# Kernel optimization log

Measured on AMD Instinct MI355X. Metric: run time of the kernel, lower is better.

## Reference

```python
import jax, jax.numpy as jnp
import numpy as np

SHIFT = 4
MARGIN = 0.15


def _shift_loss(f1, m1, f2, m2):
    # f1,f2: [B,C,H,W] float; m1,m2: [B,1,H,W] bool
    # Original repeats masks to C channels; broadcasting is equivalent,
    # but mask.sum over (1,2,3) then includes a factor of C.
    C = f1.shape[1]
    dists = []
    for i in range(2 * SHIFT + 1):
        off = -SHIFT + i
        f2r = jnp.roll(f2, off, axis=-1)
        m2r = jnp.roll(m2, off, axis=-1)
        mask = m1 & m2r                              # [B,1,H,W]
        diff = jnp.where(mask, f1 - f2r, 0.0)        # broadcast over C
        num = jnp.sum(diff * diff, axis=(1, 2, 3))   # ||.||_2^2
        den = C * jnp.sum(mask, axis=(1, 2, 3)).astype(f1.dtype) + 0.001
        dists.append(num / den)
    return jnp.min(jnp.stack(dists, axis=0), axis=0)  # min over 9 shifts -> [B]


def setup_inputs() -> dict:
    key = jax.random.key(0)
    ka, kp, kn, kma, kmp, kmn = jax.random.split(key, 6)
    B, C, H, W = 64, 16, 32, 512
    a = jax.random.normal(ka, (B, C, H, W), dtype=jnp.float32)
    p = jax.random.normal(kp, (B, C, H, W), dtype=jnp.float32)
    n = jax.random.normal(kn, (B, C, H, W), dtype=jnp.float32)
    ma = jax.random.bernoulli(kma, 0.8, (B, 1, H, W))
    mp = jax.random.bernoulli(kmp, 0.8, (B, 1, H, W))
    mn = jax.random.bernoulli(kmn, 0.8, (B, 1, H, W))
    return {"a": a, "p": p, "n": n, "ma": ma, "mp": mp, "mn": mn}


def reference(a, p, n, ma, mp, mn):
    ap_loss = _shift_loss(a, ma, p, mp)
    an_loss = _shift_loss(a, ma, n, mn)
    loss = jax.nn.relu(ap_loss - an_loss + MARGIN)
    return jnp.mean(loss)
```

## Files before the change

### kernel.cpp

```cpp
#include <hip/hip_runtime.h>

#define NB 64
#define NC 16
#define NH 32
#define NW 512
#define HW (NH * NW)
#define CHW (NC * HW)
#define NOFF 9
#define NCPB 4

#define WS_NUM_AP 0
#define WS_NUM_AN 576
#define WS_CNT_AP 1152
#define WS_CNT_AN 1728
#define WS_FLOATS 2304

__device__ __forceinline__ float wave_sum_f(float v) {
#pragma unroll
    for (int o = 32; o > 0; o >>= 1) v += __shfl_down(v, o, 64);
    return v;
}

__global__ __launch_bounds__(256, 4) void num_kernel(
    const float* __restrict__ a, const float* __restrict__ p,
    const float* __restrict__ n, const int* __restrict__ ma,
    const int* __restrict__ mp, const int* __restrict__ mn,
    float* __restrict__ ws)
{
    const int b    = blockIdx.z;
    const int pair = blockIdx.y & 1;
    const int cg   = blockIdx.y >> 1;
    const int tid  = blockIdx.x * 256 + threadIdx.x;
    const int pos0 = tid * 4;
    const int w0   = pos0 & (NW - 1);
    const int row  = pos0 - w0;
    const int idxm = row + ((w0 - 4) & (NW - 1));
    const int idxp = row + ((w0 + 4) & (NW - 1));

    const int* MA = ma + b * HW;
    const int* M2 = (pair ? mn : mp) + b * HW;
    int4 mav = *(const int4*)(MA + pos0);
    int4 mf0 = *(const int4*)(M2 + idxm);
    int4 mf1 = *(const int4*)(M2 + pos0);
    int4 mf2 = *(const int4*)(M2 + idxp);

    float m1f[4]  = {mav.x ? 1.f : 0.f, mav.y ? 1.f : 0.f,
                     mav.z ? 1.f : 0.f, mav.w ? 1.f : 0.f};
    float m2f[12] = {mf0.x ? 1.f : 0.f, mf0.y ? 1.f : 0.f, mf0.z ? 1.f : 0.f, mf0.w ? 1.f : 0.f,
                     mf1.x ? 1.f : 0.f, mf1.y ? 1.f : 0.f, mf1.z ? 1.f : 0.f, mf1.w ? 1.f : 0.f,
                     mf2.x ? 1.f : 0.f, mf2.y ? 1.f : 0.f, mf2.z ? 1.f : 0.f, mf2.w ? 1.f : 0.f};

    const float* A = a + (size_t)b * CHW + (size_t)cg * NCPB * HW;
    const float* F = (pair ? n : p) + (size_t)b * CHW + (size_t)cg * NCPB * HW;

    float sa2[4];
    float sf2[12];
    float crS[NOFF];
#pragma unroll
    for (int j = 0; j < 4; ++j) sa2[j] = 0.f;
#pragma unroll
    for (int k = 0; k < 12; ++k) sf2[k] = 0.f;
#pragma unroll
    for (int s = 0; s < NOFF; ++s) crS[s] = 0.f;

#pragma unroll 2
    for (int c = 0; c < NCPB; ++c) {
        const float* Ac = A + c * HW;
        const float* Fc = F + c * HW;

        float4 av4 = *(const float4*)(Ac + pos0);
        float fb[12];
        *(float4*)&fb[0] = *(const float4*)(Fc + idxm);
        *(float4*)&fb[4] = *(const float4*)(Fc + pos0);
        *(float4*)&fb[8] = *(const float4*)(Fc + idxp);
        float avr[4] = {av4.x, av4.y, av4.z, av4.w};

        float am[4], fm[12];
#pragma unroll
        for (int j = 0; j < 4; ++j) am[j] = avr[j] * m1f[j];
#pragma unroll
        for (int k = 0; k < 12; ++k) fm[k] = fb[k] * m2f[k];

#pragma unroll
        for (int j = 0; j < 4; ++j) sa2[j] = fmaf(am[j], am[j], sa2[j]);
#pragma unroll
        for (int k = 0; k < 12; ++k) sf2[k] = fmaf(fm[k], fm[k], sf2[k]);
#pragma unroll
        for (int s = 0; s < NOFF; ++s) {
#pragma unroll
            for (int j = 0; j < 4; ++j) {
                crS[s] = fmaf(am[j], fm[j + 8 - s], crS[s]);
            }
        }
    }

    float sx[NOFF], cxf[NOFF];
#pragma unroll
    for (int s = 0; s < NOFF; ++s) {
        float t = 0.f, cc = 0.f;
#pragma unroll
        for (int j = 0; j < 4; ++j) {
            const int k = j + 8 - s;
            t  = fmaf(m2f[k], sa2[j], t);
            t  = fmaf(m1f[j], sf2[k], t);
            cc = fmaf(m1f[j], m2f[k], cc);
        }
        sx[s]  = fmaf(-2.f, crS[s], t);
        cxf[s] = cc;
    }

    __shared__ float red[4][20];
    const int lane = threadIdx.x & 63;
    const int wid  = threadIdx.x >> 6;

#pragma unroll
    for (int s = 0; s < NOFF; ++s) sx[s] = wave_sum_f(sx[s]);
    if (cg == 0) {
#pragma unroll
        for (int s = 0; s < NOFF; ++s) cxf[s] = wave_sum_f(cxf[s]);
    }
    if (lane == 0) {
#pragma unroll
        for (int s = 0; s < NOFF; ++s) {
            red[wid][s] = sx[s];
            red[wid][9 + s] = cxf[s];
        }
    }
    __syncthreads();

    float* numws = ws + (pair ? WS_NUM_AN : WS_NUM_AP) + b * NOFF;
    float* cntws = ws + (pair ? WS_CNT_AN : WS_CNT_AP) + b * NOFF;
    const int i = threadIdx.x;
    if (i < 9) {
        float v = red[0][i] + red[1][i] + red[2][i] + red[3][i];
        atomicAdd(numws + i, v);
    } else if (i < 18 && cg == 0) {
        float v = red[0][i] + red[1][i] + red[2][i] + red[3][i];
        atomicAdd(cntws + (i - 9), v);
    }
}

__global__ void finish_kernel(const float* __restrict__ ws, float* __restrict__ out)
{
    const int b = threadIdx.x;
    const float* num_ap = ws + WS_NUM_AP;
    const float* num_an = ws + WS_NUM_AN;
    const float* cnt_ap = ws + WS_CNT_AP;
    const float* cnt_an = ws + WS_CNT_AN;

    float ap = 3.4e38f, an = 3.4e38f;
#pragma unroll
    for (int s = 0; s < NOFF; ++s) {
        ap = fminf(ap, num_ap[b * NOFF + s] / (16.f * cnt_ap[b * NOFF + s] + 0.001f));
        an = fminf(an, num_an[b * NOFF + s] / (16.f * cnt_an[b * NOFF + s] + 0.001f));
    }
    float loss = fmaxf(ap - an + 0.15f, 0.f);
    loss = wave_sum_f(loss);
    if (b == 0) out[0] = loss * (1.0f / 64.f);
}

extern "C" void kernel_launch(void* const* d_in, const int* in_sizes, int n_in,
                              void* d_out, int out_size, void* d_ws, size_t ws_size,
                              hipStream_t stream) {
    const float* a = (const float*)d_in[0];
    const float* p = (const float*)d_in[1];
    const float* n = (const float*)d_in[2];
    const int* ma = (const int*)d_in[3];
    const int* mp = (const int*)d_in[4];
    const int* mn = (const int*)d_in[5];
    float* ws = (float*)d_ws;
    float* out = (float*)d_out;

    hipMemsetAsync(d_ws, 0, WS_FLOATS * sizeof(float), stream);

    num_kernel<<<dim3(16, 8, NB), 256, 0, stream>>>(a, p, n, ma, mp, mn, ws);
    finish_kernel<<<1, 64, 0, stream>>>(ws, out);
}
```

Baseline: 209.5 us.

## Map one wave per row and share shift halos via lane shuffles

Each wave now processes a full image row with eight contiguous elements per lane. The ±4 shift neighbourhood is obtained from adjacent lanes through shuffles instead of extra overlapping global loads of the second feature map and mask. This cuts redundant memory requests and halves the grid, at the cost of more registers per thread and added shuffle instructions.

```diff
diff --git a/kernel.cpp b/kernel.cpp
--- a/kernel.cpp
+++ b/kernel.cpp
@@ -30,36 +30,31 @@
     const int b    = blockIdx.z;
     const int pair = blockIdx.y & 1;
     const int cg   = blockIdx.y >> 1;
-    const int tid  = blockIdx.x * 256 + threadIdx.x;
-    const int pos0 = tid * 4;
-    const int w0   = pos0 & (NW - 1);
-    const int row  = pos0 - w0;
-    const int idxm = row + ((w0 - 4) & (NW - 1));
-    const int idxp = row + ((w0 + 4) & (NW - 1));
+    const int lane = threadIdx.x & 63;
+    const int wid  = threadIdx.x >> 6;
+    const int row  = blockIdx.x * 4 + wid;
+    const int base = row * NW + lane * 8;
+    const int prevL = (lane + 63) & 63;
+    const int nextL = (lane + 1)  & 63;
 
-    const int* MA = ma + b * HW;
-    const int* M2 = (pair ? mn : mp) + b * HW;
-    int4 mav = *(const int4*)(MA + pos0);
-    int4 mf0 = *(const int4*)(M2 + idxm);
-    int4 mf1 = *(const int4*)(M2 + pos0);
-    int4 mf2 = *(const int4*)(M2 + idxp);
+    const int* MA = ma + b * HW + base;
+    const int* M2 = (pair ? mn : mp) + b * HW + base;
+    int4 ma0 = *(const int4*)(MA);
+    int4 ma1 = *(const int4*)(MA + 4);
+    int4 mb0 = *(const int4*)(M2);
+    int4 mb1 = *(const int4*)(M2 + 4);
 
-    float m1f[4]  = {mav.x ? 1.f : 0.f, mav.y ? 1.f : 0.f,
-                     mav.z ? 1.f : 0.f, mav.w ? 1.f : 0.f};
-    float m2f[12] = {mf0.x ? 1.f : 0.f, mf0.y ? 1.f : 0.f, mf0.z ? 1.f : 0.f, mf0.w ? 1.f : 0.f,
-                     mf1.x ? 1.f : 0.f, mf1.y ? 1.f : 0.f, mf1.z ? 1.f : 0.f, mf1.w ? 1.f : 0.f,
-                     mf2.x ? 1.f : 0.f, mf2.y ? 1.f : 0.f, mf2.z ? 1.f : 0.f, mf2.w ? 1.f : 0.f};
+    float m1f[8] = {ma0.x ? 1.f : 0.f, ma0.y ? 1.f : 0.f, ma0.z ? 1.f : 0.f, ma0.w ? 1.f : 0.f,
+                    ma1.x ? 1.f : 0.f, ma1.y ? 1.f : 0.f, ma1.z ? 1.f : 0.f, ma1.w ? 1.f : 0.f};
+    float m2f[8] = {mb0.x ? 1.f : 0.f, mb0.y ? 1.f : 0.f, mb0.z ? 1.f : 0.f, mb0.w ? 1.f : 0.f,
+                    mb1.x ? 1.f : 0.f, mb1.y ? 1.f : 0.f, mb1.z ? 1.f : 0.f, mb1.w ? 1.f : 0.f};
 
-    const float* A = a + (size_t)b * CHW + (size_t)cg * NCPB * HW;
-    const float* F = (pair ? n : p) + (size_t)b * CHW + (size_t)cg * NCPB * HW;
+    const float* A = a + (size_t)b * CHW + (size_t)cg * NCPB * HW + base;
+    const float* F = (pair ? n : p) + (size_t)b * CHW + (size_t)cg * NCPB * HW + base;
 
-    float sa2[4];
-    float sf2[12];
-    float crS[NOFF];
+    float sa2[8], sf2[8], crS[NOFF];
 #pragma unroll
-    for (int j = 0; j < 4; ++j) sa2[j] = 0.f;
-#pragma unroll
-    for (int k = 0; k < 12; ++k) sf2[k] = 0.f;
+    for (int j = 0; j < 8; ++j) { sa2[j] = 0.f; sf2[j] = 0.f; }
 #pragma unroll
     for (int s = 0; s < NOFF; ++s) crS[s] = 0.f;
 
@@ -67,31 +62,50 @@
     for (int c = 0; c < NCPB; ++c) {
         const float* Ac = A + c * HW;
         const float* Fc = F + c * HW;
+        float4 a0 = *(const float4*)(Ac);
+        float4 a1 = *(const float4*)(Ac + 4);
+        float4 f0 = *(const float4*)(Fc);
+        float4 f1 = *(const float4*)(Fc + 4);
+        float av[8] = {a0.x, a0.y, a0.z, a0.w, a1.x, a1.y, a1.z, a1.w};
+        float fv[8] = {f0.x, f0.y, f0.z, f0.w, f1.x, f1.y, f1.z, f1.w};
 
-        float4 av4 = *(const float4*)(Ac + pos0);
-        float fb[12];
-        *(float4*)&fb[0] = *(const float4*)(Fc + idxm);
-        *(float4*)&fb[4] = *(const float4*)(Fc + pos0);
-        *(float4*)&fb[8] = *(const float4*)(Fc + idxp);
-        float avr[4] = {av4.x, av4.y, av4.z, av4.w};
+        float am[8], fm[8];
+#pragma unroll
+        for (int j = 0; j < 8; ++j) { am[j] = av[j] * m1f[j]; fm[j] = fv[j] * m2f[j]; }
 
-        float am[4], fm[12];
+        float wfm[16];
 #pragma unroll
-        for (int j = 0; j < 4; ++j) am[j] = avr[j] * m1f[j];
+        for (int i = 0; i < 4; ++i) wfm[i]      = __shfl(fm[4 + i], prevL, 64);
 #pragma unroll
-        for (int k = 0; k < 12; ++k) fm[k] = fb[k] * m2f[k];
+        for (int i = 0; i < 8; ++i) wfm[4 + i]  = fm[i];
+#pragma unroll
+        for (int i = 0; i < 4; ++i) wfm[12 + i] = __shfl(fm[i], nextL, 64);
 
 #pragma unroll
-        for (int j = 0; j < 4; ++j) sa2[j] = fmaf(am[j], am[j], sa2[j]);
+        for (int j = 0; j < 8; ++j) sa2[j] = fmaf(am[j], am[j], sa2[j]);
 #pragma unroll
-        for (int k = 0; k < 12; ++k) sf2[k] = fmaf(fm[k], fm[k], sf2[k]);
+        for (int j = 0; j < 8; ++j) sf2[j] = fmaf(fm[j], fm[j], sf2[j]);
 #pragma unroll
         for (int s = 0; s < NOFF; ++s) {
 #pragma unroll
-            for (int j = 0; j < 4; ++j) {
-                crS[s] = fmaf(am[j], fm[j + 8 - s], crS[s]);
+            for (int j = 0; j < 8; ++j) {
+                crS[s] = fmaf(am[j], wfm[j + 8 - s], crS[s]);
             }
         }
+    }
+
+    float sf2w[16], m2w[16];
+#pragma unroll
+    for (int i = 0; i < 4; ++i) {
+        sf2w[i]      = __shfl(sf2[4 + i], prevL, 64);
+        m2w[i]       = __shfl(m2f[4 + i], prevL, 64);
+    }
+#pragma unroll
+    for (int i = 0; i < 8; ++i) { sf2w[4 + i] = sf2[i]; m2w[4 + i] = m2f[i]; }
+#pragma unroll
+    for (int i = 0; i < 4; ++i) {
+        sf2w[12 + i] = __shfl(sf2[i], nextL, 64);
+        m2w[12 + i]  = __shfl(m2f[i], nextL, 64);
     }
 
     float sx[NOFF], cxf[NOFF];
@@ -99,20 +113,17 @@
     for (int s = 0; s < NOFF; ++s) {
         float t = 0.f, cc = 0.f;
 #pragma unroll
-        for (int j = 0; j < 4; ++j) {
+        for (int j = 0; j < 8; ++j) {
             const int k = j + 8 - s;
-            t  = fmaf(m2f[k], sa2[j], t);
-            t  = fmaf(m1f[j], sf2[k], t);
-            cc = fmaf(m1f[j], m2f[k], cc);
+            t  = fmaf(m2w[k], sa2[j], t);
+            t  = fmaf(m1f[j], sf2w[k], t);
+            cc = fmaf(m1f[j], m2w[k], cc);
         }
         sx[s]  = fmaf(-2.f, crS[s], t);
         cxf[s] = cc;
     }
 
     __shared__ float red[4][20];
-    const int lane = threadIdx.x & 63;
-    const int wid  = threadIdx.x >> 6;
-
 #pragma unroll
     for (int s = 0; s < NOFF; ++s) sx[s] = wave_sum_f(sx[s]);
     if (cg == 0) {
@@ -173,6 +184,6 @@
 
     hipMemsetAsync(d_ws, 0, WS_FLOATS * sizeof(float), stream);
 
-    num_kernel<<<dim3(16, 8, NB), 256, 0, stream>>>(a, p, n, ma, mp, mn, ws);
+    num_kernel<<<dim3(8, 8, NB), 256, 0, stream>>>(a, p, n, ma, mp, mn, ws);
     finish_kernel<<<1, 64, 0, stream>>>(ws, out);
 }
```

Result: slower. 215.8 us (+3.0%).
